# Kernel optimization log

Hardware: AMD Instinct MI355X
Metric: run time of the kernel (lower is better)

The kernel has to match this reference:

```python
import jax, jax.numpy as jnp
import numpy as np

G = 5            # semantic groups: head_spine, left_arm, right_arm, left_leg, right_leg
B = 131072       # batch of pose samples
K = 512          # tokens_per_group
D = 64           # token_dim
COMMITMENT_COST = 0.25


def setup_inputs() -> dict:
    key = jax.random.key(0)
    k1, k2 = jax.random.split(key)
    features = jax.random.normal(k1, (G, B, D), dtype=jnp.float32)
    # nn.Embedding init: uniform(-1/num_embeddings, 1/num_embeddings)
    codebooks = jax.random.uniform(k2, (G, K, D), dtype=jnp.float32,
                                   minval=-1.0 / K, maxval=1.0 / K)
    return {"features": features, "codebooks": codebooks}


def reference(features, codebooks):
    """features: [G, B, D], codebooks: [G, K, D].
    Returns (quantized [G,B,D], per_group_loss [G], total_loss scalar, indices [G,B]).
    """
    x_sq = jnp.sum(features ** 2, axis=-1, keepdims=True)          # [G, B, 1]
    e_sq = jnp.sum(codebooks ** 2, axis=-1)[:, None, :]            # [G, 1, K]
    cross = jnp.einsum('gbd,gkd->gbk', features, codebooks)        # [G, B, K]
    distances = x_sq + e_sq - 2.0 * cross

    indices = jnp.argmin(distances, axis=-1)                       # [G, B]
    # gather codebook rows (replaces one-hot scatter + matmul)
    quantized = jnp.take_along_axis(codebooks, indices[:, :, None], axis=1)  # [G, B, D]

    # per-group MSE losses (straight-through VQ loss)
    e_latent = jnp.mean((jax.lax.stop_gradient(quantized) - features) ** 2, axis=(1, 2))
    q_latent = jnp.mean((quantized - jax.lax.stop_gradient(features)) ** 2, axis=(1, 2))
    per_group_loss = q_latent + COMMITMENT_COST * e_latent          # [G]
    total_loss = jnp.sum(per_group_loss)

    # straight-through estimator
    quantized_st = features + jax.lax.stop_gradient(quantized - features)
    return quantized_st, per_group_loss, total_loss, indices
```

## Files before the change

### kernel.cpp

```cpp
#include <hip/hip_runtime.h>

typedef _Float16 half8 __attribute__((ext_vector_type(8)));
typedef float floatx16 __attribute__((ext_vector_type(16)));

constexpr int Gn = 5;
constexpr int Bn = 131072;
constexpr int Kn = 512;
constexpr int Dn = 64;

constexpr long long QOFF = (long long)Gn * Bn * Dn;
constexpr long long IOFF = QOFF + Gn + 1;
constexpr unsigned CAPE = 49152;

__global__ void vq_esq(const float* __restrict__ code, float* __restrict__ esq) {
    int i = blockIdx.x * blockDim.x + threadIdx.x;
    if (i >= Gn * Kn) return;
    const float4* c4 = reinterpret_cast<const float4*>(code + (long long)i * Dn);
    float s0 = 0.f, s1 = 0.f, s2 = 0.f, s3 = 0.f;
#pragma unroll
    for (int j = 0; j < 16; ++j) {
        float4 v = c4[j];
        s0 += v.x * v.x; s1 += v.y * v.y; s2 += v.z * v.z; s3 += v.w * v.w;
    }
    esq[i] = (s0 + s1) + (s2 + s3);
}

__global__ void vq_cvt(const float* __restrict__ code, const float* __restrict__ esq,
                       _Float16* __restrict__ ch16, _Float16* __restrict__ cl16,
                       float* __restrict__ cbias) {
    int i = blockIdx.x * blockDim.x + threadIdx.x;
    if (i < Gn * Kn * Dn) {
        float v = code[i];
        _Float16 h = (_Float16)v;
        ch16[i] = h;
        cl16[i] = (_Float16)((v - (float)h) * 2048.0f);
    }
    if (i < Gn * Kn) cbias[i] = 1.0f + 0.5f * esq[i];
}

__global__ __launch_bounds__(256, 2) void vq_screen(
    const float* __restrict__ feat, const float* __restrict__ codef,
    const _Float16* __restrict__ ch16, const _Float16* __restrict__ cl16,
    const float* __restrict__ cbias, float* __restrict__ out,
    float* __restrict__ acc, unsigned* __restrict__ cnt,
    unsigned* __restrict__ entries)
{
    const int g = blockIdx.y;
    const int lane = threadIdx.x & 63;
    const int wv = threadIdx.x >> 6;
    const int l31 = lane & 31;
    const int hh = lane >> 5;
    const long long rowbase = (long long)blockIdx.x * 256 + wv * 64;
    const float MARGIN = 4.0e-5f;

    half8 aH[2][4], aL[2][4];
    float xsq_p[2];
    const float* fg = feat + ((long long)g * Bn + rowbase) * Dn;
#pragma unroll
    for (int t = 0; t < 2; ++t) {
        const float* rp = fg + (long long)(t * 32 + l31) * Dn + hh * 8;
        float xs = 0.f;
#pragma unroll
        for (int s = 0; s < 4; ++s) {
            float4 u0 = *(const float4*)(rp + 16 * s);
            float4 u1 = *(const float4*)(rp + 16 * s + 4);
            half8 h, l;
            h[0] = (_Float16)u0.x; h[1] = (_Float16)u0.y;
            h[2] = (_Float16)u0.z; h[3] = (_Float16)u0.w;
            h[4] = (_Float16)u1.x; h[5] = (_Float16)u1.y;
            h[6] = (_Float16)u1.z; h[7] = (_Float16)u1.w;
            l[0] = (_Float16)((u0.x - (float)h[0]) * 2048.0f);
            l[1] = (_Float16)((u0.y - (float)h[1]) * 2048.0f);
            l[2] = (_Float16)((u0.z - (float)h[2]) * 2048.0f);
            l[3] = (_Float16)((u0.w - (float)h[3]) * 2048.0f);
            l[4] = (_Float16)((u1.x - (float)h[4]) * 2048.0f);
            l[5] = (_Float16)((u1.y - (float)h[5]) * 2048.0f);
            l[6] = (_Float16)((u1.z - (float)h[6]) * 2048.0f);
            l[7] = (_Float16)((u1.w - (float)h[7]) * 2048.0f);
            aH[t][s] = h; aL[t][s] = l;
            xs += u0.x*u0.x + u0.y*u0.y + u0.z*u0.z + u0.w*u0.w
                + u1.x*u1.x + u1.y*u1.y + u1.z*u1.z + u1.w*u1.w;
        }
        xs += __shfl_xor(xs, 32);
        xsq_p[t] = xs;
    }

    float v1[2][16], v2[2][16];
#pragma unroll
    for (int t = 0; t < 2; ++t)
#pragma unroll
        for (int r = 0; r < 16; ++r) { v1[t][r] = 3.0e38f; v2[t][r] = 3.0e38f; }

    const _Float16* bbh = ch16 + ((long long)g * Kn + l31) * Dn + hh * 8;
    const _Float16* bbl = cl16 + ((long long)g * Kn + l31) * Dn + hh * 8;
    half8 bH[4], bL[4];
#pragma unroll
    for (int s = 0; s < 4; ++s) {
        bH[s] = *(const half8*)(bbh + 16 * s);
        bL[s] = *(const half8*)(bbl + 16 * s);
    }

    for (int ch = 0; ch < 16; ++ch) {
        float c = cbias[g * Kn + ch * 32 + l31];
        half8 nH[4], nL[4];
        if (ch < 15) {
            const _Float16* ph = bbh + (long long)(ch + 1) * 32 * Dn;
            const _Float16* pl = bbl + (long long)(ch + 1) * 32 * Dn;
#pragma unroll
            for (int s = 0; s < 4; ++s) {
                nH[s] = *(const half8*)(ph + 16 * s);
                nL[s] = *(const half8*)(pl + 16 * s);
            }
        }
        floatx16 h0 = {0.f}, h1 = {0.f}, lo0 = {0.f}, lo1 = {0.f};
#pragma unroll
        for (int s = 0; s < 4; ++s) {
            h0  = __builtin_amdgcn_mfma_f32_32x32x16_f16(aH[0][s], bH[s], h0, 0, 0, 0);
            h1  = __builtin_amdgcn_mfma_f32_32x32x16_f16(aH[1][s], bH[s], h1, 0, 0, 0);
            lo0 = __builtin_amdgcn_mfma_f32_32x32x16_f16(aL[0][s], bH[s], lo0, 0, 0, 0);
            lo1 = __builtin_amdgcn_mfma_f32_32x32x16_f16(aL[1][s], bH[s], lo1, 0, 0, 0);
        }
#pragma unroll
        for (int s = 0; s < 4; ++s) {
            lo0 = __builtin_amdgcn_mfma_f32_32x32x16_f16(aH[0][s], bL[s], lo0, 0, 0, 0);
            lo1 = __builtin_amdgcn_mfma_f32_32x32x16_f16(aH[1][s], bL[s], lo1, 0, 0, 0);
        }
#pragma unroll
        for (int r = 0; r < 16; ++r) {
            float cd0 = (c - h0[r]) - 4.8828125e-4f * lo0[r];
            cd0 = __int_as_float((__float_as_int(cd0) & ~15) | ch);
            v2[0][r] = fminf(v2[0][r], fmaxf(v1[0][r], cd0));
            v1[0][r] = fminf(v1[0][r], cd0);
            float cd1 = (c - h1[r]) - 4.8828125e-4f * lo1[r];
            cd1 = __int_as_float((__float_as_int(cd1) & ~15) | ch);
            v2[1][r] = fminf(v2[1][r], fmaxf(v1[1][r], cd1));
            v1[1][r] = fminf(v1[1][r], cd1);
        }
        if (ch < 15) {
#pragma unroll
            for (int s = 0; s < 4; ++s) { bH[s] = nH[s]; bL[s] = nL[s]; }
        }
    }

    int col[2][16];
#pragma unroll
    for (int t = 0; t < 2; ++t)
#pragma unroll
        for (int r = 0; r < 16; ++r)
            col[t][r] = ((__float_as_int(v1[t][r]) & 15) << 5) + l31;

#pragma unroll
    for (int mi = 0; mi < 5; ++mi) {
        const int m = 1 << mi;
#pragma unroll
        for (int t = 0; t < 2; ++t)
#pragma unroll
            for (int r = 0; r < 16; ++r) {
                float ov1 = __shfl_xor(v1[t][r], m);
                float ov2 = __shfl_xor(v2[t][r], m);
                int   oc  = __shfl_xor(col[t][r], m);
                float mx = fmaxf(v1[t][r], ov1);
                v2[t][r] = fminf(fminf(v2[t][r], ov2), mx);
                if (ov1 < v1[t][r]) { v1[t][r] = ov1; col[t][r] = oc; }
            }
    }

    float lsum = 0.f;
    bool fl[2] = {false, false};
    unsigned rw[2] = {0u, 0u};
#pragma unroll
    for (int t = 0; t < 2; ++t) {
#pragma unroll
        for (int r = 0; r < 16; ++r) {
            const int ra = (r & 3) + 8 * (r >> 2) + 4 * hh;
            const long long grow = rowbase + t * 32 + ra;
            const int cc = col[t][r];
            const float* qsrc = codef + ((long long)(g * Kn + cc)) * Dn;
            float2 qv = *(const float2*)(qsrc + 2 * l31);
            *(float2*)(out + ((long long)g * Bn + grow) * Dn + 2 * l31) = qv;
            if (l31 == ra) {
                out[IOFF + (long long)g * Bn + grow] = (float)cc;
                float v1c = __int_as_float(__float_as_int(v1[t][r]) & ~15);
                float v2c = __int_as_float(__float_as_int(v2[t][r]) & ~15);
                lsum += xsq_p[t] + 2.0f * (v1c - 1.0f);
                fl[t] = (v2c - v1c <= MARGIN);
                rw[t] = (unsigned)grow;
            }
        }
    }

    unsigned long long m0 = __ballot(fl[0]);
    unsigned long long m1 = __ballot(fl[1]);
    unsigned tot = (unsigned)(__builtin_popcountll(m0) + __builtin_popcountll(m1));
    if (tot) {
        unsigned base = 0;
        if (lane == 0) base = atomicAdd(cnt, tot);
        base = (unsigned)__shfl((int)base, 0);
        unsigned long long lt = ((unsigned long long)1 << lane) - 1;
        if (fl[0]) {
            unsigned s = base + (unsigned)__builtin_popcountll(m0 & lt);
            if (s < CAPE) entries[s] = ((unsigned)g << 17) | rw[0];
        }
        if (fl[1]) {
            unsigned s = base + (unsigned)__builtin_popcountll(m0)
                              + (unsigned)__builtin_popcountll(m1 & lt);
            if (s < CAPE) entries[s] = ((unsigned)g << 17) | rw[1];
        }
    }
#pragma unroll
    for (int m = 1; m < 64; m <<= 1) lsum += __shfl_xor(lsum, m);
    if (lane == 0) atomicAdd(&acc[g], lsum);
}

__global__ __launch_bounds__(256) void vq_rescue(
    const float* __restrict__ feat, const float* __restrict__ codef,
    const float* __restrict__ esq, const unsigned* __restrict__ cnt,
    const unsigned* __restrict__ entries, float* __restrict__ out)
{
    const int lane = threadIdx.x & 63;
    const int wid = blockIdx.x * 4 + (threadIdx.x >> 6);
    const int nw = gridDim.x * 4;
    const int n = (int)min(*cnt, CAPE);

    for (int i = wid; i < n; i += nw) {
        unsigned e = entries[i];
        int g = e >> 17;
        long long b = e & 131071u;

        const float* xp = feat + ((long long)g * Bn + b) * Dn;
        float x[64];
#pragma unroll
        for (int j = 0; j < 16; ++j) {
            float4 u = ((const float4*)xp)[j];
            x[4*j] = u.x; x[4*j+1] = u.y; x[4*j+2] = u.z; x[4*j+3] = u.w;
        }
        float xsq;
        {
#pragma clang fp contract(off)
            float r0[8];
#pragma unroll
            for (int j = 0; j < 8; ++j) r0[j] = x[j] * x[j];
#pragma unroll
            for (int q = 8; q < 64; q += 8)
#pragma unroll
                for (int j = 0; j < 8; ++j) {
                    float s0 = x[q + j] * x[q + j];
                    r0[j] = r0[j] + s0;
                }
            xsq = ((r0[0] + r0[1]) + (r0[2] + r0[3])) + ((r0[4] + r0[5]) + (r0[6] + r0[7]));
        }

        const float* cg = codef + (long long)g * Kn * Dn;
        const float* eg = esq + g * Kn;
        float best = 3.4e38f; int bk = 0x7fffffff;
        for (int j = 0; j < 8; ++j) {
            int k = j * 64 + lane;
            const float4* cp = (const float4*)(cg + (long long)k * Dn);
            float d0 = 0.f, d1 = 0.f, d2 = 0.f, d3 = 0.f;
#pragma unroll
            for (int q = 0; q < 16; ++q) {
                float4 v = cp[q];
                d0 = fmaf(v.x, x[4*q+0], d0);
                d1 = fmaf(v.y, x[4*q+1], d1);
                d2 = fmaf(v.z, x[4*q+2], d2);
                d3 = fmaf(v.w, x[4*q+3], d3);
            }
            float dot = (d0 + d1) + (d2 + d3);
            float dist = (xsq + eg[k]) - 2.0f * dot;
            if (dist < best) { best = dist; bk = k; }
        }
#pragma unroll
        for (int m = 1; m < 64; m <<= 1) {
            float ov = __shfl_xor(best, m);
            int   ok = __shfl_xor(bk, m);
            if (ov < best || (ov == best && ok < bk)) { best = ov; bk = ok; }
        }
        if (lane == 0) out[IOFF + (long long)g * Bn + b] = (float)bk;
        out[((long long)g * Bn + b) * Dn + lane] = cg[(long long)bk * Dn + lane];
    }
}

__global__ void vq_finalize(const float* __restrict__ acc, float* __restrict__ out) {
    if (threadIdx.x == 0 && blockIdx.x == 0) {
        float tot = 0.f;
#pragma unroll
        for (int g = 0; g < Gn; ++g) {
            float m = acc[g] / 8388608.0f;
            float l = m + 0.25f * m;
            out[QOFF + g] = l;
            tot += l;
        }
        out[QOFF + Gn] = tot;
    }
}

extern "C" void kernel_launch(void* const* d_in, const int* in_sizes, int n_in,
                              void* d_out, int out_size, void* d_ws, size_t ws_size,
                              hipStream_t stream) {
    const float* feat = (const float*)d_in[0];
    const float* code = (const float*)d_in[1];
    float* out = (float*)d_out;

    char* w = (char*)d_ws;
    float*     acc     = (float*)w;
    unsigned*  cnt     = (unsigned*)(w + 64);
    float*     esq     = (float*)(w + 128);
    float*     cbias   = (float*)(w + 10368);
    _Float16*  ch16    = (_Float16*)(w + 20608);
    _Float16*  cl16    = (_Float16*)(w + 348288);
    unsigned*  entries = (unsigned*)(w + 675968);

    hipMemsetAsync(w, 0, 128, stream);
    vq_esq<<<(Gn * Kn + 255) / 256, 256, 0, stream>>>(code, esq);
    vq_cvt<<<(Gn * Kn * Dn + 255) / 256, 256, 0, stream>>>(code, esq, ch16, cl16, cbias);
    dim3 grid(Bn / 256, Gn);
    vq_screen<<<grid, 256, 0, stream>>>(feat, code, ch16, cl16, cbias, out, acc, cnt, entries);
    vq_rescue<<<2048, 256, 0, stream>>>(feat, code, esq, cnt, entries, out);
    vq_finalize<<<1, 64, 0, stream>>>(acc, out);
}
```

Before: 650.0 us.

## Restructure VQ screening with transposed MFMA, folded bias and fewer kernels

Restructures the screen kernel so each wave handles 32 rows with the codebook as the MFMA A-operand. Each lane then tracks a single running top-2 across its column instead of 32 per-register top-2 pairs, which removes the five-stage shuffle reduction. The feature low-part MFMAs are dropped, leaving only the codebook low residual. The -0.5||e||^2 bias is folded in through an extra MFMA with a one-hot operand, and the reduction uses fmed3. Codebook prep kernels are merged and finalize is folded into rescue to cut launches. The extra fp16 precision loss, from dropping the feature low part and storing the bias in fp16, is meant to be covered by a slightly wider rescue margin, which risks more rows going to the rescue path.

```diff
diff --git a/kernel.cpp b/kernel.cpp
--- a/kernel.cpp
+++ b/kernel.cpp
@@ -12,37 +12,38 @@
 constexpr long long IOFF = QOFF + Gn + 1;
 constexpr unsigned CAPE = 49152;
 
-__global__ void vq_esq(const float* __restrict__ code, float* __restrict__ esq) {
+__global__ void vq_prep(const float* __restrict__ code, float* __restrict__ esq,
+                        _Float16* __restrict__ ch16, _Float16* __restrict__ cl16,
+                        _Float16* __restrict__ esqh) {
     int i = blockIdx.x * blockDim.x + threadIdx.x;
     if (i >= Gn * Kn) return;
     const float4* c4 = reinterpret_cast<const float4*>(code + (long long)i * Dn);
+    _Float16* hp = ch16 + (long long)i * Dn;
+    _Float16* lp = cl16 + (long long)i * Dn;
     float s0 = 0.f, s1 = 0.f, s2 = 0.f, s3 = 0.f;
 #pragma unroll
     for (int j = 0; j < 16; ++j) {
         float4 v = c4[j];
         s0 += v.x * v.x; s1 += v.y * v.y; s2 += v.z * v.z; s3 += v.w * v.w;
-    }
-    esq[i] = (s0 + s1) + (s2 + s3);
-}
-
-__global__ void vq_cvt(const float* __restrict__ code, const float* __restrict__ esq,
-                       _Float16* __restrict__ ch16, _Float16* __restrict__ cl16,
-                       float* __restrict__ cbias) {
-    int i = blockIdx.x * blockDim.x + threadIdx.x;
-    if (i < Gn * Kn * Dn) {
-        float v = code[i];
-        _Float16 h = (_Float16)v;
-        ch16[i] = h;
-        cl16[i] = (_Float16)((v - (float)h) * 2048.0f);
-    }
-    if (i < Gn * Kn) cbias[i] = 1.0f + 0.5f * esq[i];
-}
-
-__global__ __launch_bounds__(256, 2) void vq_screen(
+        _Float16 hx = (_Float16)v.x, hy = (_Float16)v.y;
+        _Float16 hz = (_Float16)v.z, hw = (_Float16)v.w;
+        hp[4 * j + 0] = hx; hp[4 * j + 1] = hy;
+        hp[4 * j + 2] = hz; hp[4 * j + 3] = hw;
+        lp[4 * j + 0] = (_Float16)((v.x - (float)hx) * 2048.0f);
+        lp[4 * j + 1] = (_Float16)((v.y - (float)hy) * 2048.0f);
+        lp[4 * j + 2] = (_Float16)((v.z - (float)hz) * 2048.0f);
+        lp[4 * j + 3] = (_Float16)((v.w - (float)hw) * 2048.0f);
+    }
+    float e = (s0 + s1) + (s2 + s3);
+    esq[i] = e;
+    esqh[i] = (_Float16)(-(e * 1024.0f));
+}
+
+__global__ __launch_bounds__(256, 3) void vq_screen(
     const float* __restrict__ feat, const float* __restrict__ codef,
     const _Float16* __restrict__ ch16, const _Float16* __restrict__ cl16,
-    const float* __restrict__ cbias, float* __restrict__ out,
-    float* __restrict__ acc, unsigned* __restrict__ cnt,
+    const _Float16* __restrict__ esqh, float* __restrict__ out,
+    float* __restrict__ accg, unsigned* __restrict__ cnt,
     unsigned* __restrict__ entries)
 {
     const int g = blockIdx.y;
@@ -50,173 +51,146 @@
     const int wv = threadIdx.x >> 6;
     const int l31 = lane & 31;
     const int hh = lane >> 5;
-    const long long rowbase = (long long)blockIdx.x * 256 + wv * 64;
-    const float MARGIN = 4.0e-5f;
-
-    half8 aH[2][4], aL[2][4];
-    float xsq_p[2];
-    const float* fg = feat + ((long long)g * Bn + rowbase) * Dn;
-#pragma unroll
-    for (int t = 0; t < 2; ++t) {
-        const float* rp = fg + (long long)(t * 32 + l31) * Dn + hh * 8;
-        float xs = 0.f;
-#pragma unroll
-        for (int s = 0; s < 4; ++s) {
-            float4 u0 = *(const float4*)(rp + 16 * s);
-            float4 u1 = *(const float4*)(rp + 16 * s + 4);
-            half8 h, l;
-            h[0] = (_Float16)u0.x; h[1] = (_Float16)u0.y;
-            h[2] = (_Float16)u0.z; h[3] = (_Float16)u0.w;
-            h[4] = (_Float16)u1.x; h[5] = (_Float16)u1.y;
-            h[6] = (_Float16)u1.z; h[7] = (_Float16)u1.w;
-            l[0] = (_Float16)((u0.x - (float)h[0]) * 2048.0f);
-            l[1] = (_Float16)((u0.y - (float)h[1]) * 2048.0f);
-            l[2] = (_Float16)((u0.z - (float)h[2]) * 2048.0f);
-            l[3] = (_Float16)((u0.w - (float)h[3]) * 2048.0f);
-            l[4] = (_Float16)((u1.x - (float)h[4]) * 2048.0f);
-            l[5] = (_Float16)((u1.y - (float)h[5]) * 2048.0f);
-            l[6] = (_Float16)((u1.z - (float)h[6]) * 2048.0f);
-            l[7] = (_Float16)((u1.w - (float)h[7]) * 2048.0f);
-            aH[t][s] = h; aL[t][s] = l;
-            xs += u0.x*u0.x + u0.y*u0.y + u0.z*u0.z + u0.w*u0.w
-                + u1.x*u1.x + u1.y*u1.y + u1.z*u1.z + u1.w*u1.w;
-        }
-        xs += __shfl_xor(xs, 32);
-        xsq_p[t] = xs;
-    }
-
-    float v1[2][16], v2[2][16];
-#pragma unroll
-    for (int t = 0; t < 2; ++t)
-#pragma unroll
-        for (int r = 0; r < 16; ++r) { v1[t][r] = 3.0e38f; v2[t][r] = 3.0e38f; }
-
-    const _Float16* bbh = ch16 + ((long long)g * Kn + l31) * Dn + hh * 8;
-    const _Float16* bbl = cl16 + ((long long)g * Kn + l31) * Dn + hh * 8;
-    half8 bH[4], bL[4];
+    const long long rowbase = (long long)blockIdx.x * 128 + wv * 32;
+    const float MARGIN = 5.0e-5f;
+    const int CLR = (int)0xFFFFFF00;
+
+    half8 fH[4], fHs[4];
+    const float* rp = feat + ((long long)g * Bn + rowbase + l31) * Dn + hh * 8;
+    float xs = 0.f;
 #pragma unroll
     for (int s = 0; s < 4; ++s) {
-        bH[s] = *(const half8*)(bbh + 16 * s);
-        bL[s] = *(const half8*)(bbl + 16 * s);
-    }
+        float4 u0 = *(const float4*)(rp + 16 * s);
+        float4 u1 = *(const float4*)(rp + 16 * s + 4);
+        half8 h;
+        h[0] = (_Float16)u0.x; h[1] = (_Float16)u0.y;
+        h[2] = (_Float16)u0.z; h[3] = (_Float16)u0.w;
+        h[4] = (_Float16)u1.x; h[5] = (_Float16)u1.y;
+        h[6] = (_Float16)u1.z; h[7] = (_Float16)u1.w;
+        fH[s] = h;
+        fHs[s] = h * (_Float16)4.8828125e-4f;
+        xs += u0.x*u0.x + u0.y*u0.y + u0.z*u0.z + u0.w*u0.w
+            + u1.x*u1.x + u1.y*u1.y + u1.z*u1.z + u1.w*u1.w;
+    }
+    xs += __shfl_xor(xs, 32);
+
+    half8 b5 = {(_Float16)0.f};
+    b5[0] = hh ? (_Float16)0.f : (_Float16)4.8828125e-4f;
+
+    const _Float16* bh = ch16 + ((long long)g * Kn + l31) * Dn + hh * 8;
+    const _Float16* bl = cl16 + ((long long)g * Kn + l31) * Dn + hh * 8;
+    const _Float16* ep = esqh + g * Kn + l31;
+
+    half8 cH[4], cLs[4];
+#pragma unroll
+    for (int s = 0; s < 4; ++s) {
+        cH[s]  = *(const half8*)(bh + 16 * s);
+        cLs[s] = *(const half8*)(bl + 16 * s);
+    }
+    _Float16 a5v = ep[0];
+
+    float v1 = -3.0e38f, v2 = -3.0e38f;
 
     for (int ch = 0; ch < 16; ++ch) {
-        float c = cbias[g * Kn + ch * 32 + l31];
-        half8 nH[4], nL[4];
+        half8 nH[4], nLs[4];
+        _Float16 na5 = (_Float16)0.f;
         if (ch < 15) {
-            const _Float16* ph = bbh + (long long)(ch + 1) * 32 * Dn;
-            const _Float16* pl = bbl + (long long)(ch + 1) * 32 * Dn;
+            const _Float16* ph = bh + (ch + 1) * 2048;
+            const _Float16* pl = bl + (ch + 1) * 2048;
 #pragma unroll
             for (int s = 0; s < 4; ++s) {
-                nH[s] = *(const half8*)(ph + 16 * s);
-                nL[s] = *(const half8*)(pl + 16 * s);
+                nH[s]  = *(const half8*)(ph + 16 * s);
+                nLs[s] = *(const half8*)(pl + 16 * s);
             }
-        }
-        floatx16 h0 = {0.f}, h1 = {0.f}, lo0 = {0.f}, lo1 = {0.f};
-#pragma unroll
-        for (int s = 0; s < 4; ++s) {
-            h0  = __builtin_amdgcn_mfma_f32_32x32x16_f16(aH[0][s], bH[s], h0, 0, 0, 0);
-            h1  = __builtin_amdgcn_mfma_f32_32x32x16_f16(aH[1][s], bH[s], h1, 0, 0, 0);
-            lo0 = __builtin_amdgcn_mfma_f32_32x32x16_f16(aL[0][s], bH[s], lo0, 0, 0, 0);
-            lo1 = __builtin_amdgcn_mfma_f32_32x32x16_f16(aL[1][s], bH[s], lo1, 0, 0, 0);
-        }
-#pragma unroll
-        for (int s = 0; s < 4; ++s) {
-            lo0 = __builtin_amdgcn_mfma_f32_32x32x16_f16(aH[0][s], bL[s], lo0, 0, 0, 0);
-            lo1 = __builtin_amdgcn_mfma_f32_32x32x16_f16(aH[1][s], bL[s], lo1, 0, 0, 0);
-        }
+            na5 = ep[(ch + 1) * 32];
+        }
+        half8 a5 = {(_Float16)0.f};
+        a5[0] = hh ? (_Float16)0.f : a5v;
+
+        floatx16 acc = {0.f};
+#pragma unroll
+        for (int s = 0; s < 4; ++s)
+            acc = __builtin_amdgcn_mfma_f32_32x32x16_f16(cH[s], fH[s], acc, 0, 0, 0);
+#pragma unroll
+        for (int s = 0; s < 4; ++s)
+            acc = __builtin_amdgcn_mfma_f32_32x32x16_f16(cLs[s], fHs[s], acc, 0, 0, 0);
+        acc = __builtin_amdgcn_mfma_f32_32x32x16_f16(a5, b5, acc, 0, 0, 0);
+
+        const int idb = ch << 4;
 #pragma unroll
         for (int r = 0; r < 16; ++r) {
-            float cd0 = (c - h0[r]) - 4.8828125e-4f * lo0[r];
-            cd0 = __int_as_float((__float_as_int(cd0) & ~15) | ch);
-            v2[0][r] = fminf(v2[0][r], fmaxf(v1[0][r], cd0));
-            v1[0][r] = fminf(v1[0][r], cd0);
-            float cd1 = (c - h1[r]) - 4.8828125e-4f * lo1[r];
-            cd1 = __int_as_float((__float_as_int(cd1) & ~15) | ch);
-            v2[1][r] = fminf(v2[1][r], fmaxf(v1[1][r], cd1));
-            v1[1][r] = fminf(v1[1][r], cd1);
+            float cd = __int_as_float((__float_as_int(acc[r]) & CLR) | (idb | r));
+            v2 = __builtin_amdgcn_fmed3f(v1, v2, cd);
+            v1 = fmaxf(v1, cd);
         }
         if (ch < 15) {
 #pragma unroll
-            for (int s = 0; s < 4; ++s) { bH[s] = nH[s]; bL[s] = nL[s]; }
-        }
-    }
-
-    int col[2][16];
-#pragma unroll
-    for (int t = 0; t < 2; ++t)
-#pragma unroll
-        for (int r = 0; r < 16; ++r)
-            col[t][r] = ((__float_as_int(v1[t][r]) & 15) << 5) + l31;
-
-#pragma unroll
-    for (int mi = 0; mi < 5; ++mi) {
-        const int m = 1 << mi;
-#pragma unroll
-        for (int t = 0; t < 2; ++t)
-#pragma unroll
-            for (int r = 0; r < 16; ++r) {
-                float ov1 = __shfl_xor(v1[t][r], m);
-                float ov2 = __shfl_xor(v2[t][r], m);
-                int   oc  = __shfl_xor(col[t][r], m);
-                float mx = fmaxf(v1[t][r], ov1);
-                v2[t][r] = fminf(fminf(v2[t][r], ov2), mx);
-                if (ov1 < v1[t][r]) { v1[t][r] = ov1; col[t][r] = oc; }
-            }
-    }
+            for (int s = 0; s < 4; ++s) { cH[s] = nH[s]; cLs[s] = nLs[s]; }
+            a5v = na5;
+        }
+    }
+
+    float o1 = __shfl_xor(v1, 32);
+    float o2 = __shfl_xor(v2, 32);
+    float w1 = fmaxf(v1, o1);
+    float w2 = fmaxf(fminf(v1, o1), fmaxf(v2, o2));
+    int hsrc = (o1 > v1) ? (hh ^ 1) : hh;
+    int idw = __float_as_int(w1) & 255;
+    int rr  = idw & 15;
+    int code = ((idw >> 4) << 5) + (rr & 3) + 8 * (rr >> 2) + 4 * hsrc;
+    float v1c = __int_as_float(__float_as_int(w1) & CLR);
+    float v2c = __int_as_float(__float_as_int(w2) & CLR);
+
+    const long long grow = rowbase + l31;
+    const float* qsrc = codef + ((long long)(g * Kn + code)) * Dn + hh * 32;
+    float* qdst = out + ((long long)g * Bn + grow) * Dn + hh * 32;
+#pragma unroll
+    for (int q = 0; q < 8; ++q)
+        *(float4*)(qdst + 4 * q) = *(const float4*)(qsrc + 4 * q);
 
     float lsum = 0.f;
-    bool fl[2] = {false, false};
-    unsigned rw[2] = {0u, 0u};
-#pragma unroll
-    for (int t = 0; t < 2; ++t) {
-#pragma unroll
-        for (int r = 0; r < 16; ++r) {
-            const int ra = (r & 3) + 8 * (r >> 2) + 4 * hh;
-            const long long grow = rowbase + t * 32 + ra;
-            const int cc = col[t][r];
-            const float* qsrc = codef + ((long long)(g * Kn + cc)) * Dn;
-            float2 qv = *(const float2*)(qsrc + 2 * l31);
-            *(float2*)(out + ((long long)g * Bn + grow) * Dn + 2 * l31) = qv;
-            if (l31 == ra) {
-                out[IOFF + (long long)g * Bn + grow] = (float)cc;
-                float v1c = __int_as_float(__float_as_int(v1[t][r]) & ~15);
-                float v2c = __int_as_float(__float_as_int(v2[t][r]) & ~15);
-                lsum += xsq_p[t] + 2.0f * (v1c - 1.0f);
-                fl[t] = (v2c - v1c <= MARGIN);
-                rw[t] = (unsigned)grow;
-            }
-        }
-    }
-
-    unsigned long long m0 = __ballot(fl[0]);
-    unsigned long long m1 = __ballot(fl[1]);
-    unsigned tot = (unsigned)(__builtin_popcountll(m0) + __builtin_popcountll(m1));
+    bool fl = false;
+    if (hh == 0) {
+        out[IOFF + (long long)g * Bn + grow] = (float)code;
+        lsum = xs - 2.0f * v1c;
+        fl = (v1c - v2c <= MARGIN);
+    }
+
+    unsigned long long m0 = __ballot(fl);
+    unsigned tot = (unsigned)__builtin_popcountll(m0);
     if (tot) {
         unsigned base = 0;
         if (lane == 0) base = atomicAdd(cnt, tot);
         base = (unsigned)__shfl((int)base, 0);
-        unsigned long long lt = ((unsigned long long)1 << lane) - 1;
-        if (fl[0]) {
+        if (fl) {
+            unsigned long long lt = ((unsigned long long)1 << lane) - 1;
             unsigned s = base + (unsigned)__builtin_popcountll(m0 & lt);
-            if (s < CAPE) entries[s] = ((unsigned)g << 17) | rw[0];
-        }
-        if (fl[1]) {
-            unsigned s = base + (unsigned)__builtin_popcountll(m0)
-                              + (unsigned)__builtin_popcountll(m1 & lt);
-            if (s < CAPE) entries[s] = ((unsigned)g << 17) | rw[1];
+            if (s < CAPE) entries[s] = ((unsigned)g << 17) | (unsigned)grow;
         }
     }
 #pragma unroll
     for (int m = 1; m < 64; m <<= 1) lsum += __shfl_xor(lsum, m);
-    if (lane == 0) atomicAdd(&acc[g], lsum);
+    if (lane == 0) atomicAdd(&accg[g], lsum);
 }
 
 __global__ __launch_bounds__(256) void vq_rescue(
     const float* __restrict__ feat, const float* __restrict__ codef,
     const float* __restrict__ esq, const unsigned* __restrict__ cnt,
-    const unsigned* __restrict__ entries, float* __restrict__ out)
+    const unsigned* __restrict__ entries, float* __restrict__ out,
+    const float* __restrict__ accg)
 {
+    if (blockIdx.x == 0 && threadIdx.x == 0) {
+        float tot = 0.f;
+#pragma unroll
+        for (int g = 0; g < Gn; ++g) {
+            float m = accg[g] / 8388608.0f;
+            float l = m + 0.25f * m;
+            out[QOFF + g] = l;
+            tot += l;
+        }
+        out[QOFF + Gn] = tot;
+    }
+
     const int lane = threadIdx.x & 63;
     const int wid = blockIdx.x * 4 + (threadIdx.x >> 6);
     const int nw = gridDim.x * 4;
@@ -280,20 +254,6 @@
     }
 }
 
-__global__ void vq_finalize(const float* __restrict__ acc, float* __restrict__ out) {
-    if (threadIdx.x == 0 && blockIdx.x == 0) {
-        float tot = 0.f;
-#pragma unroll
-        for (int g = 0; g < Gn; ++g) {
-            float m = acc[g] / 8388608.0f;
-            float l = m + 0.25f * m;
-            out[QOFF + g] = l;
-            tot += l;
-        }
-        out[QOFF + Gn] = tot;
-    }
-}
-
 extern "C" void kernel_launch(void* const* d_in, const int* in_sizes, int n_in,
                               void* d_out, int out_size, void* d_ws, size_t ws_size,
                               hipStream_t stream) {
@@ -305,16 +265,14 @@
     float*     acc     = (float*)w;
     unsigned*  cnt     = (unsigned*)(w + 64);
     float*     esq     = (float*)(w + 128);
-    float*     cbias   = (float*)(w + 10368);
-    _Float16*  ch16    = (_Float16*)(w + 20608);
-    _Float16*  cl16    = (_Float16*)(w + 348288);
-    unsigned*  entries = (unsigned*)(w + 675968);
+    _Float16*  esqh    = (_Float16*)(w + 10368);
+    _Float16*  ch16    = (_Float16*)(w + 15488);
+    _Float16*  cl16    = (_Float16*)(w + 343168);
+    unsigned*  entries = (unsigned*)(w + 670848);
 
     hipMemsetAsync(w, 0, 128, stream);
-    vq_esq<<<(Gn * Kn + 255) / 256, 256, 0, stream>>>(code, esq);
-    vq_cvt<<<(Gn * Kn * Dn + 255) / 256, 256, 0, stream>>>(code, esq, ch16, cl16, cbias);
-    dim3 grid(Bn / 256, Gn);
-    vq_screen<<<grid, 256, 0, stream>>>(feat, code, ch16, cl16, cbias, out, acc, cnt, entries);
-    vq_rescue<<<2048, 256, 0, stream>>>(feat, code, esq, cnt, entries, out);
-    vq_finalize<<<1, 64, 0, stream>>>(acc, out);
-}
+    vq_prep<<<(Gn * Kn + 255) / 256, 256, 0, stream>>>(code, esq, ch16, cl16, esqh);
+    dim3 grid(Bn / 128, Gn);
+    vq_screen<<<grid, 256, 0, stream>>>(feat, code, ch16, cl16, esqh, out, acc, cnt, entries);
+    vq_rescue<<<2048, 256, 0, stream>>>(feat, code, esq, cnt, entries, out, acc);
+}
```

Measured after the change: 779.0 us. 1.2x slower.
